# Optimization experiments

Hardware: AMD Instinct MI355X
Metric: run time of the kernel (lower is better)

## Reference

```python
import jax, jax.numpy as jnp
import numpy as np

DIM, NH, NKV, HD = 4096, 32, 8, 128
B, KV_LEN, WINDOW = 32, 4096, 4096
G = NH // NKV  # q heads per kv head (GQA group)


def setup_inputs() -> dict:
    key = jax.random.key(0)
    ks = jax.random.split(key, 7)
    s = 1.0 / np.sqrt(DIM)
    return {
        "x": jax.random.normal(ks[0], (1, 1, B, DIM), jnp.float32),
        "wqkv": jax.random.normal(ks[1], (DIM, DIM + 2 * NKV * HD), jnp.float32) * s,
        "wo": jax.random.normal(ks[2], (DIM, DIM), jnp.float32) * s,
        "rot_mat": jax.random.normal(ks[3], (HD, HD), jnp.float32) * (1.0 / np.sqrt(HD)),
        "cache_k": jax.random.normal(ks[4], (B, NKV, KV_LEN, HD), jnp.float32),
        "cache_v": jax.random.normal(ks[5], (B, NKV, KV_LEN, HD), jnp.float32),
        "attn_mask": jnp.zeros((1, NH, B, WINDOW), jnp.float32),
        "current_pos": 4095,
    }


def reference(x, wqkv, wo, rot_mat, cache_k, cache_v, attn_mask, current_pos):
    # fused QKV projection: (1,1,B,DIM) @ (DIM,6144) -> (1,1,B,6144)
    xqkv = x @ wqkv
    q = xqkv[..., : NH * HD].reshape(1, 1, B, NH, HD)
    k = xqkv[..., NH * HD : (NH + NKV) * HD].reshape(1, 1, B, NKV, HD)
    v = xqkv[..., (NH + NKV) * HD :].reshape(1, 1, B, NKV, HD)
    # nlp_create_qkv_heads layout: (seq, n_heads, batch, head_dim)
    q = jnp.transpose(q[:, 0], (0, 2, 1, 3))  # (1, NH, B, HD)
    k = jnp.transpose(k[:, 0], (0, 2, 1, 3))  # (1, NKV, B, HD)
    v = jnp.transpose(v[:, 0], (0, 2, 1, 3))  # (1, NKV, B, HD)
    # RoPE as matmul on last dim
    q = q @ rot_mat
    k = k @ rot_mat
    # KV-cache update at current_pos: cache is (B, NKV, KV_LEN, HD)
    cache_k = cache_k.at[:, :, current_pos, :].set(jnp.transpose(k[0], (1, 0, 2)))
    cache_v = cache_v.at[:, :, current_pos, :].set(jnp.transpose(v[0], (1, 0, 2)))
    # unpad valid region (padded to nearest 32, capped by sliding window)
    L = min(((current_pos + 1 + 31) // 32) * 32, WINDOW)
    keys = cache_k[:, :, :L]    # (B, NKV, L, HD)
    values = cache_v[:, :, :L]  # (B, NKV, L, HD)
    # grouped attention: q (1, NKV, G, B, HD) vs keys (B, NKV, L, HD)
    qg = q.reshape(1, NKV, G, B, HD)
    scores = jnp.einsum("qkgbd,bkld->qkgbl", qg, keys)  # (1,NKV,G,B,L)
    scores = scores.reshape(1, NH, B, L) / jnp.sqrt(jnp.float32(HD))
    scores = scores + attn_mask[..., :L]
    probs = jax.nn.softmax(scores, axis=-1)
    out = jnp.einsum("qkgbl,bkld->qkgbd", probs.reshape(1, NKV, G, B, L), values)
    out = out.reshape(1, NH, B, HD)
    # concatenate heads -> (1,1,B,DIM)
    out = jnp.transpose(out, (0, 2, 1, 3)).reshape(1, 1, B, NH * HD)
    return out @ wo
```

## Files before the change

### kernel.cpp

```cpp
#include <hip/hip_runtime.h>

#define BB 32
#define DIM 4096
#define NH 32
#define NKV 8
#define HD 128
#define KVLEN 4096
#define QKVC 6144
#define GQ 4
#define QKV_SPLITS 32
#define WO_SPLITS 32
#define ASPLIT 2
#define NT 32

typedef const __attribute__((address_space(1))) char gas_char;
typedef __attribute__((address_space(3))) char las_char;
#define GLL16(GP, LP) __builtin_amdgcn_global_load_lds((gas_char*)(GP), (las_char*)(LP), 16, 0, 0)

__global__ __launch_bounds__(256, 4) void k_qkv(const float* __restrict__ x,
                                                const float* __restrict__ w,
                                                float* __restrict__ part) {
    int j  = blockIdx.x * 256 + threadIdx.x;
    int d0 = blockIdx.y * (DIM / QKV_SPLITS);
    float acc[BB];
#pragma unroll
    for (int b = 0; b < BB; ++b) acc[b] = 0.f;
    for (int dd = d0; dd < d0 + DIM / QKV_SPLITS; dd += 16) {
        float wr[16];
#pragma unroll
        for (int k = 0; k < 16; ++k) wr[k] = w[(size_t)(dd + k) * QKVC + j];
#pragma unroll
        for (int b = 0; b < BB; ++b) {
            float4 xa = *(const float4*)&x[b * DIM + dd];
            float4 xb = *(const float4*)&x[b * DIM + dd + 4];
            float4 xc = *(const float4*)&x[b * DIM + dd + 8];
            float4 xd = *(const float4*)&x[b * DIM + dd + 12];
            float t = acc[b];
            t = fmaf(xa.x, wr[0],  t); t = fmaf(xa.y, wr[1],  t);
            t = fmaf(xa.z, wr[2],  t); t = fmaf(xa.w, wr[3],  t);
            t = fmaf(xb.x, wr[4],  t); t = fmaf(xb.y, wr[5],  t);
            t = fmaf(xb.z, wr[6],  t); t = fmaf(xb.w, wr[7],  t);
            t = fmaf(xc.x, wr[8],  t); t = fmaf(xc.y, wr[9],  t);
            t = fmaf(xc.z, wr[10], t); t = fmaf(xc.w, wr[11], t);
            t = fmaf(xd.x, wr[12], t); t = fmaf(xd.y, wr[13], t);
            t = fmaf(xd.z, wr[14], t); t = fmaf(xd.w, wr[15], t);
            acc[b] = t;
        }
    }
#pragma unroll
    for (int b = 0; b < BB; ++b)
        part[(size_t)blockIdx.y * (BB * QKVC) + (size_t)b * QKVC + j] = acc[b];
}

__global__ __launch_bounds__(256) void k_red(const float* __restrict__ src,
                                             float* __restrict__ dst,
                                             int parts, int n4) {
    int i = blockIdx.x * 256 + threadIdx.x;
    if (i >= n4) return;
    const float4* s4 = (const float4*)src;
    float4 a = s4[i];
    for (int p = 1; p < parts; ++p) {
        float4 b = s4[(size_t)p * n4 + i];
        a.x += b.x; a.y += b.y; a.z += b.z; a.w += b.w;
    }
    ((float4*)dst)[i] = a;
}

__global__ __launch_bounds__(128) void k_rot(const float* __restrict__ xqkv,
                                             const float* __restrict__ rot,
                                             float* __restrict__ qws,
                                             float* __restrict__ kws) {
    int c  = blockIdx.x;
    int b  = blockIdx.y;
    int dp = threadIdx.x;
    const float* row = &xqkv[(size_t)b * QKVC + c * HD];
    float acc = 0.f;
#pragma unroll 4
    for (int d = 0; d < HD; ++d) acc = fmaf(row[d], rot[d * HD + dp], acc);
    if (c < 32) {
        qws[((size_t)b * NH + c) * HD + dp] = acc;
    } else {
        int kvh = c - 32;
        kws[((size_t)b * NKV + kvh) * HD + dp] = acc;
    }
}

__global__ __launch_bounds__(256, 2) void k_attn(const float* __restrict__ ck,
                                                 const float* __restrict__ cv,
                                                 const float* __restrict__ qws,
                                                 const float* __restrict__ kws,
                                                 const float* __restrict__ xqkv,
                                                 const float* __restrict__ mask,
                                                 const int* __restrict__ curpos,
                                                 float* __restrict__ opart,
                                                 float2* __restrict__ stats) {
    __shared__ float Kl[2][64 * 128];
    __shared__ float mbuf[2][GQ * 64];
    __shared__ float ql[GQ][HD];
    __shared__ float pl[GQ * 64];
    __shared__ float rs[GQ];
    int bkv = blockIdx.x;
    int split = blockIdx.y;
    int b = bkv >> 3, kv = bkv & 7;
    int tid = threadIdx.x;
    int wv = tid >> 6, lane = tid & 63;
    int d4 = tid & 31, sub = tid >> 5;
    int lrh = lane >> 5;
    int sbyte = (lane & 31) << 4;
    int pos = *curpos;
    int L = min((((pos + 1) + 31) >> 5) << 5, KVLEN);
    int l0 = split * (NT * 64);
    int h = kv * GQ + wv;
    const float scale = 0.08838834764831845f;

    *(float2*)&ql[wv][lane * 2] = *(const float2*)&qws[((size_t)b * NH + h) * HD + lane * 2];

    float posdot = 0.f;
    {
        const float4* kwr = (const float4*)&kws[((size_t)b * NKV + kv) * HD];
        const float4* qr  = (const float4*)&qws[((size_t)b * NH + h) * HD];
#pragma unroll
        for (int i = 0; i < 32; ++i) {
            float4 a = kwr[i], c = qr[i];
            posdot += a.x * c.x + a.y * c.y + a.z * c.z + a.w * c.w;
        }
    }
    float4 vnew4 = *(const float4*)&xqkv[(size_t)b * QKVC + (size_t)(NH + NKV) * HD + kv * HD + d4 * 4];

    const char*   Ktile0 = (const char*)(ck + ((size_t)bkv * KVLEN + l0) * HD);
    const float4* Vt0    = (const float4*)(cv + ((size_t)bkv * KVLEN + l0) * HD);

#define STAGE_K(T, BUFI) do {                                                    \
        const char* kb_ = Ktile0 + (size_t)(T) * 32768;                          \
        _Pragma("unroll")                                                        \
        for (int i_ = 0; i_ < 8; ++i_) {                                         \
            int row_ = (i_ * 4 + wv) * 2 + lrh;                                  \
            int col_ = sbyte ^ ((row_ & 31) << 4);                               \
            GLL16(kb_ + (size_t)row_ * 512 + col_, &Kl[BUFI][(i_ * 4 + wv) * 256]); \
        }                                                                        \
    } while (0)

#define STAGE_M(T, BUFI) do {                                                    \
        int hh_ = lane >> 4, kk_ = lane & 15;                                    \
        const float* mg_ = mask + (((size_t)(kv * GQ + hh_) * BB + b) * KVLEN    \
                                   + l0 + (T) * 64 + kk_ * 4);                   \
        GLL16(mg_, &mbuf[BUFI][0]);                                              \
    } while (0)

    float m = -3.0e38f, lsum = 0.f;
    float4 acc[GQ];
#pragma unroll
    for (int gg = 0; gg < GQ; ++gg) acc[gg] = make_float4(0.f, 0.f, 0.f, 0.f);
    float4 vA[8], vB[8];

    STAGE_K(0, 0);
    if (wv == 0) STAGE_M(0, 0);
#pragma unroll
    for (int i = 0; i < 8; ++i) vA[i] = Vt0[(size_t)(sub * 8 + i) * 32 + d4];

#define TILE(T, BUFI, VC, VN) do {                                               \
        if ((T) < NT - 1) {                                                      \
            STAGE_K((T) + 1, (BUFI) ^ 1);                                        \
            if (wv == 0) STAGE_M((T) + 1, (BUFI) ^ 1);                           \
            _Pragma("unroll")                                                    \
            for (int i_ = 0; i_ < 8; ++i_)                                       \
                (VN)[i_] = Vt0[(size_t)(((T) + 1) * 64 + sub * 8 + i_) * 32 + d4]; \
            if (wv == 0) asm volatile("s_waitcnt vmcnt(17)" ::: "memory");       \
            else         asm volatile("s_waitcnt vmcnt(16)" ::: "memory");       \
        } else {                                                                 \
            asm volatile("s_waitcnt vmcnt(0)" ::: "memory");                     \
        }                                                                        \
        __builtin_amdgcn_s_barrier();                                            \
                                                   \
        int lk_ = l0 + (T) * 64 + lane;                                          \
        const char* klr_ = (const char*)&Kl[BUFI][0] + lane * 512;               \
        float sdot_ = 0.f;                                                       \
        _Pragma("unroll")                                                        \
        for (int dd_ = 0; dd_ < 32; ++dd_) {                                     \
            float4 kk4_ = *(const float4*)(klr_ + ((dd_ * 16) ^ sbyte));         \
            float4 qq4_ = *(const float4*)&ql[wv][dd_ * 4];                      \
            sdot_ += kk4_.x * qq4_.x + kk4_.y * qq4_.y                           \
                   + kk4_.z * qq4_.z + kk4_.w * qq4_.w;                          \
        }                                                                        \
        if (lk_ == pos) sdot_ = posdot;                                          \
        float s_ = sdot_ * scale + mbuf[BUFI][wv * 64 + lane];                   \
        if (lk_ >= L) s_ = -3.0e38f;                                             \
        float smax_ = s_;                                                        \
        _Pragma("unroll")                                                        \
        for (int off_ = 32; off_ > 0; off_ >>= 1)                                \
            smax_ = fmaxf(smax_, __shfl_xor(smax_, off_));                       \
        float mnew_ = fmaxf(m, smax_);                                           \
        float r_ = __expf(m - mnew_);                                            \
        float e_ = (lk_ < L) ? __expf(s_ - mnew_) : 0.f;                         \
        float esum_ = e_;                                                        \
        _Pragma("unroll")                                                        \
        for (int off_ = 32; off_ > 0; off_ >>= 1)                                \
            esum_ += __shfl_xor(esum_, off_);                                    \
        lsum = lsum * r_ + esum_;                                                \
        m = mnew_;                                                               \
        pl[wv * 64 + lane] = e_;                                                 \
        if (lane == 0) rs[wv] = r_;                                              \
        asm volatile("s_waitcnt lgkmcnt(0)" ::: "memory");                       \
        __builtin_amdgcn_s_barrier();                                            \
                              \
        int prow_ = pos - (l0 + (T) * 64);                                       \
        _Pragma("unroll")                                                        \
        for (int gg_ = 0; gg_ < GQ; ++gg_) {                                     \
            float rg_ = rs[gg_];                                                 \
            acc[gg_].x *= rg_; acc[gg_].y *= rg_;                                \
            acc[gg_].z *= rg_; acc[gg_].w *= rg_;                                \
        }                                                                        \
        _Pragma("unroll")                                                        \
        for (int i_ = 0; i_ < 8; ++i_) {                                         \
            float4 v_ = (sub * 8 + i_ == prow_) ? vnew4 : (VC)[i_];              \
            _Pragma("unroll")                                                    \
            for (int gg_ = 0; gg_ < GQ; ++gg_) {                                 \
                float p_ = pl[gg_ * 64 + sub * 8 + i_];                          \
                acc[gg_].x = fmaf(p_, v_.x, acc[gg_].x);                         \
                acc[gg_].y = fmaf(p_, v_.y, acc[gg_].y);                         \
                acc[gg_].z = fmaf(p_, v_.z, acc[gg_].z);                         \
                acc[gg_].w = fmaf(p_, v_.w, acc[gg_].w);                         \
            }                                                                    \
        }                                                                        \
    } while (0)

    for (int tt = 0; tt < NT; tt += 2) {
        TILE(tt,     0, vA, vB);
        TILE(tt + 1, 1, vB, vA);
    }

    if (lane == 0) stats[(bkv * GQ + wv) * ASPLIT + split] = make_float2(m, lsum);

    __syncthreads();
    float* red = &Kl[0][0];
#pragma unroll
    for (int gg = 0; gg < GQ; ++gg)
        *(float4*)&red[(sub * GQ + gg) * HD + d4 * 4] = acc[gg];
    __syncthreads();
#pragma unroll
    for (int rep = 0; rep < 2; ++rep) {
        int idx = rep * 256 + tid;
        int g2 = idx >> 7, d = idx & 127;
        float o = 0.f;
#pragma unroll
        for (int k = 0; k < 8; ++k) o += red[(k * GQ + g2) * HD + d];
        opart[(((size_t)split * 256 + bkv) * GQ + g2) * HD + d] = o;
    }
#undef TILE
#undef STAGE_K
#undef STAGE_M
}

__global__ __launch_bounds__(128) void k_merge(const float* __restrict__ opart,
                                               const float2* __restrict__ stats,
                                               float* __restrict__ attn) {
    int bkv = blockIdx.x;
    int d = threadIdx.x;
    int b = bkv >> 3, kv = bkv & 7;
#pragma unroll
    for (int g = 0; g < GQ; ++g) {
        float2 st[ASPLIT];
        float M = -3.0e38f;
#pragma unroll
        for (int s = 0; s < ASPLIT; ++s) {
            st[s] = stats[(bkv * GQ + g) * ASPLIT + s];
            M = fmaxf(M, st[s].x);
        }
        float Ltot = 0.f;
        float w[ASPLIT];
#pragma unroll
        for (int s = 0; s < ASPLIT; ++s) {
            w[s] = __expf(st[s].x - M);
            Ltot += st[s].y * w[s];
        }
        float inv = Ltot > 0.f ? 1.f / Ltot : 0.f;
        float o = 0.f;
#pragma unroll
        for (int s = 0; s < ASPLIT; ++s)
            o += opart[(((size_t)s * 256 + bkv) * GQ + g) * HD + d] * (w[s] * inv);
        attn[(size_t)b * DIM + (kv * GQ + g) * HD + d] = o;
    }
}

__global__ __launch_bounds__(256, 4) void k_wo(const float* __restrict__ attn,
                                               const float* __restrict__ wo,
                                               float* __restrict__ part) {
    int j  = blockIdx.x * 256 + threadIdx.x;
    int d0 = blockIdx.y * (DIM / WO_SPLITS);
    float acc[BB];
#pragma unroll
    for (int b = 0; b < BB; ++b) acc[b] = 0.f;
    for (int dd = d0; dd < d0 + DIM / WO_SPLITS; dd += 8) {
        float wr[8];
#pragma unroll
        for (int k = 0; k < 8; ++k) wr[k] = wo[(size_t)(dd + k) * DIM + j];
#pragma unroll
        for (int b = 0; b < BB; ++b) {
            float4 xa = *(const float4*)&attn[b * DIM + dd];
            float4 xb = *(const float4*)&attn[b * DIM + dd + 4];
            float t = acc[b];
            t = fmaf(xa.x, wr[0], t); t = fmaf(xa.y, wr[1], t);
            t = fmaf(xa.z, wr[2], t); t = fmaf(xa.w, wr[3], t);
            t = fmaf(xb.x, wr[4], t); t = fmaf(xb.y, wr[5], t);
            t = fmaf(xb.z, wr[6], t); t = fmaf(xb.w, wr[7], t);
            acc[b] = t;
        }
    }
#pragma unroll
    for (int b = 0; b < BB; ++b)
        part[(size_t)blockIdx.y * (BB * DIM) + (size_t)b * DIM + j] = acc[b];
}

extern "C" void kernel_launch(void* const* d_in, const int* in_sizes, int n_in,
                              void* d_out, int out_size, void* d_ws, size_t ws_size,
                              hipStream_t stream) {
    const float* x    = (const float*)d_in[0];
    const float* wqkv = (const float*)d_in[1];
    const float* wo   = (const float*)d_in[2];
    const float* rot  = (const float*)d_in[3];
    const float* ck   = (const float*)d_in[4];
    const float* cv   = (const float*)d_in[5];
    const float* mask = (const float*)d_in[6];
    const int* curpos = (const int*)d_in[7];
    float* out        = (float*)d_out;

    char* ws = (char*)d_ws;
    float*  xqkv_part = (float*)(ws);
    float*  xqkv      = (float*)(ws + 25165824);
    float*  qws       = (float*)(ws + 25952256);
    float*  kws       = (float*)(ws + 26476544);
    float*  opart     = (float*)(ws + 26607616);
    float2* stats     = (float2*)(ws + 28704768);
    float*  attn      = (float*)(ws + 28737536);
    float*  out_part  = (float*)(ws + 29261824);

    k_qkv  <<<dim3(QKVC / 256, QKV_SPLITS), 256, 0, stream>>>(x, wqkv, xqkv_part);
    k_red  <<<dim3(192),                    256, 0, stream>>>(xqkv_part, xqkv, QKV_SPLITS, BB * QKVC / 4);
    k_rot  <<<dim3(40, BB),                 128, 0, stream>>>(xqkv, rot, qws, kws);
    k_attn <<<dim3(BB * NKV, ASPLIT),       256, 0, stream>>>(ck, cv, qws, kws, xqkv, mask, curpos, opart, stats);
    k_merge<<<dim3(BB * NKV),               128, 0, stream>>>(opart, stats, attn);
    k_wo   <<<dim3(DIM / 256, WO_SPLITS),   256, 0, stream>>>(attn, wo, out_part);
    k_red  <<<dim3(128),                    256, 0, stream>>>(out_part, out, WO_SPLITS, BB * DIM / 4);
}
```

Before: 1.318 ms.

## Double attention block to 512 threads, splitting QK dot across wave pairs

The attention kernel now launches 512 threads per block. Each head's score dot product is split across two waves, each handling half of the head dimension, and the partials are combined through shared memory. Only four waves run the softmax, and K staging and V loads are spread over eight waves with half the per-thread register buffers. The aim is more memory-level parallelism and latency hiding for the bandwidth-bound KV-cache stream, at the cost of an extra barrier per tile and idle waves during softmax.

```diff
diff --git a/kernel.cpp b/kernel.cpp
--- a/kernel.cpp
+++ b/kernel.cpp
@@ -85,7 +85,7 @@
     }
 }
 
-__global__ __launch_bounds__(256, 2) void k_attn(const float* __restrict__ ck,
+__global__ __launch_bounds__(512, 4) void k_attn(const float* __restrict__ ck,
                                                  const float* __restrict__ cv,
                                                  const float* __restrict__ qws,
                                                  const float* __restrict__ kws,
@@ -97,28 +97,31 @@
     __shared__ float Kl[2][64 * 128];
     __shared__ float mbuf[2][GQ * 64];
     __shared__ float ql[GQ][HD];
+    __shared__ float pA[GQ][2][64];
     __shared__ float pl[GQ * 64];
     __shared__ float rs[GQ];
     int bkv = blockIdx.x;
     int split = blockIdx.y;
     int b = bkv >> 3, kv = bkv & 7;
     int tid = threadIdx.x;
-    int wv = tid >> 6, lane = tid & 63;
+    int w8 = tid >> 6, lane = tid & 63;
+    int hq = w8 >> 1, hf = w8 & 1;
+    int hf16 = hf * 16;
     int d4 = tid & 31, sub = tid >> 5;
     int lrh = lane >> 5;
     int sbyte = (lane & 31) << 4;
     int pos = *curpos;
     int L = min((((pos + 1) + 31) >> 5) << 5, KVLEN);
     int l0 = split * (NT * 64);
-    int h = kv * GQ + wv;
     const float scale = 0.08838834764831845f;
 
-    *(float2*)&ql[wv][lane * 2] = *(const float2*)&qws[((size_t)b * NH + h) * HD + lane * 2];
-
+    ql[tid >> 7][tid & 127] = qws[((size_t)b * NH + kv * GQ) * HD + tid];
+
+    int hp = w8 & 3;
     float posdot = 0.f;
     {
         const float4* kwr = (const float4*)&kws[((size_t)b * NKV + kv) * HD];
-        const float4* qr  = (const float4*)&qws[((size_t)b * NH + h) * HD];
+        const float4* qr  = (const float4*)&qws[((size_t)b * NH + kv * GQ + hp) * HD];
 #pragma unroll
         for (int i = 0; i < 32; ++i) {
             float4 a = kwr[i], c = qr[i];
@@ -133,10 +136,10 @@
 #define STAGE_K(T, BUFI) do {                                                    \
         const char* kb_ = Ktile0 + (size_t)(T) * 32768;                          \
         _Pragma("unroll")                                                        \
-        for (int i_ = 0; i_ < 8; ++i_) {                                         \
-            int row_ = (i_ * 4 + wv) * 2 + lrh;                                  \
+        for (int i_ = 0; i_ < 4; ++i_) {                                         \
+            int row_ = w8 * 8 + i_ * 2 + lrh;                                    \
             int col_ = sbyte ^ ((row_ & 31) << 4);                               \
-            GLL16(kb_ + (size_t)row_ * 512 + col_, &Kl[BUFI][(i_ * 4 + wv) * 256]); \
+            GLL16(kb_ + (size_t)row_ * 512 + col_, &Kl[BUFI][(w8 * 8 + i_ * 2) * 128]); \
         }                                                                        \
     } while (0)
 
@@ -147,61 +150,73 @@
         GLL16(mg_, &mbuf[BUFI][0]);                                              \
     } while (0)
 
+#define LOADV(T, VBUF) do {                                                      \
+        _Pragma("unroll")                                                        \
+        for (int i_ = 0; i_ < 4; ++i_)                                           \
+            (VBUF)[i_] = Vt0[(size_t)((T) * 64 + sub * 4 + i_) * 32 + d4];       \
+    } while (0)
+
     float m = -3.0e38f, lsum = 0.f;
     float4 acc[GQ];
 #pragma unroll
     for (int gg = 0; gg < GQ; ++gg) acc[gg] = make_float4(0.f, 0.f, 0.f, 0.f);
-    float4 vA[8], vB[8];
+    float4 vA[4], vB[4];
 
     STAGE_K(0, 0);
-    if (wv == 0) STAGE_M(0, 0);
-#pragma unroll
-    for (int i = 0; i < 8; ++i) vA[i] = Vt0[(size_t)(sub * 8 + i) * 32 + d4];
+    if (w8 == 0) STAGE_M(0, 0);
+    LOADV(0, vA);
+    asm volatile("s_waitcnt lgkmcnt(0)" ::: "memory");
 
 #define TILE(T, BUFI, VC, VN) do {                                               \
         if ((T) < NT - 1) {                                                      \
             STAGE_K((T) + 1, (BUFI) ^ 1);                                        \
-            if (wv == 0) STAGE_M((T) + 1, (BUFI) ^ 1);                           \
-            _Pragma("unroll")                                                    \
-            for (int i_ = 0; i_ < 8; ++i_)                                       \
-                (VN)[i_] = Vt0[(size_t)(((T) + 1) * 64 + sub * 8 + i_) * 32 + d4]; \
-            if (wv == 0) asm volatile("s_waitcnt vmcnt(17)" ::: "memory");       \
-            else         asm volatile("s_waitcnt vmcnt(16)" ::: "memory");       \
+            if (w8 == 0) STAGE_M((T) + 1, (BUFI) ^ 1);                           \
+            LOADV((T) + 1, VN);                                                  \
+            if (w8 == 0) asm volatile("s_waitcnt vmcnt(9)" ::: "memory");        \
+            else         asm volatile("s_waitcnt vmcnt(8)" ::: "memory");        \
         } else {                                                                 \
             asm volatile("s_waitcnt vmcnt(0)" ::: "memory");                     \
         }                                                                        \
-        __builtin_amdgcn_s_barrier();                                            \
-                                                   \
+        __builtin_amdgcn_s_barrier();                     \
+                           \
         int lk_ = l0 + (T) * 64 + lane;                                          \
         const char* klr_ = (const char*)&Kl[BUFI][0] + lane * 512;               \
-        float sdot_ = 0.f;                                                       \
-        _Pragma("unroll")                                                        \
-        for (int dd_ = 0; dd_ < 32; ++dd_) {                                     \
+        float pd_ = 0.f;                                                         \
+        _Pragma("unroll")                                                        \
+        for (int j_ = 0; j_ < 16; ++j_) {                                        \
+            int dd_ = hf16 + j_;                                                 \
             float4 kk4_ = *(const float4*)(klr_ + ((dd_ * 16) ^ sbyte));         \
-            float4 qq4_ = *(const float4*)&ql[wv][dd_ * 4];                      \
-            sdot_ += kk4_.x * qq4_.x + kk4_.y * qq4_.y                           \
-                   + kk4_.z * qq4_.z + kk4_.w * qq4_.w;                          \
-        }                                                                        \
-        if (lk_ == pos) sdot_ = posdot;                                          \
-        float s_ = sdot_ * scale + mbuf[BUFI][wv * 64 + lane];                   \
-        if (lk_ >= L) s_ = -3.0e38f;                                             \
-        float smax_ = s_;                                                        \
-        _Pragma("unroll")                                                        \
-        for (int off_ = 32; off_ > 0; off_ >>= 1)                                \
-            smax_ = fmaxf(smax_, __shfl_xor(smax_, off_));                       \
-        float mnew_ = fmaxf(m, smax_);                                           \
-        float r_ = __expf(m - mnew_);                                            \
-        float e_ = (lk_ < L) ? __expf(s_ - mnew_) : 0.f;                         \
-        float esum_ = e_;                                                        \
-        _Pragma("unroll")                                                        \
-        for (int off_ = 32; off_ > 0; off_ >>= 1)                                \
-            esum_ += __shfl_xor(esum_, off_);                                    \
-        lsum = lsum * r_ + esum_;                                                \
-        m = mnew_;                                                               \
-        pl[wv * 64 + lane] = e_;                                                 \
-        if (lane == 0) rs[wv] = r_;                                              \
+            float4 qq4_ = *(const float4*)&ql[hq][dd_ * 4];                      \
+            pd_ += kk4_.x * qq4_.x + kk4_.y * qq4_.y                             \
+                 + kk4_.z * qq4_.z + kk4_.w * qq4_.w;                            \
+        }                                                                        \
+        pA[hq][hf][lane] = pd_;                                                  \
         asm volatile("s_waitcnt lgkmcnt(0)" ::: "memory");                       \
-        __builtin_amdgcn_s_barrier();                                            \
+        __builtin_amdgcn_s_barrier();                  \
+                  \
+        if (w8 < 4) {                                                            \
+            float sdot_ = pA[w8][0][lane] + pA[w8][1][lane];                     \
+            if (lk_ == pos) sdot_ = posdot;                                      \
+            float s_ = sdot_ * scale + mbuf[BUFI][w8 * 64 + lane];               \
+            if (lk_ >= L) s_ = -3.0e38f;                                         \
+            float smax_ = s_;                                                    \
+            _Pragma("unroll")                                                    \
+            for (int off_ = 32; off_ > 0; off_ >>= 1)                            \
+                smax_ = fmaxf(smax_, __shfl_xor(smax_, off_));                   \
+            float mnew_ = fmaxf(m, smax_);                                       \
+            float r_ = __expf(m - mnew_);                                        \
+            float e_ = (lk_ < L) ? __expf(s_ - mnew_) : 0.f;                     \
+            float esum_ = e_;                                                    \
+            _Pragma("unroll")                                                    \
+            for (int off_ = 32; off_ > 0; off_ >>= 1)                            \
+                esum_ += __shfl_xor(esum_, off_);                                \
+            lsum = lsum * r_ + esum_;                                            \
+            m = mnew_;                                                           \
+            pl[w8 * 64 + lane] = e_;                                             \
+            if (lane == 0) rs[w8] = r_;                                          \
+        }                                                                        \
+        asm volatile("s_waitcnt lgkmcnt(0)" ::: "memory");                       \
+        __builtin_amdgcn_s_barrier();                     \
                               \
         int prow_ = pos - (l0 + (T) * 64);                                       \
         _Pragma("unroll")                                                        \
@@ -211,11 +226,11 @@
             acc[gg_].z *= rg_; acc[gg_].w *= rg_;                                \
         }                                                                        \
         _Pragma("unroll")                                                        \
-        for (int i_ = 0; i_ < 8; ++i_) {                                         \
-            float4 v_ = (sub * 8 + i_ == prow_) ? vnew4 : (VC)[i_];              \
+        for (int i_ = 0; i_ < 4; ++i_) {                                         \
+            float4 v_ = (sub * 4 + i_ == prow_) ? vnew4 : (VC)[i_];              \
             _Pragma("unroll")                                                    \
             for (int gg_ = 0; gg_ < GQ; ++gg_) {                                 \
-                float p_ = pl[gg_ * 64 + sub * 8 + i_];                          \
+                float p_ = pl[gg_ * 64 + sub * 4 + i_];                          \
                 acc[gg_].x = fmaf(p_, v_.x, acc[gg_].x);                         \
                 acc[gg_].y = fmaf(p_, v_.y, acc[gg_].y);                         \
                 acc[gg_].z = fmaf(p_, v_.z, acc[gg_].z);                         \
@@ -229,7 +244,8 @@
         TILE(tt + 1, 1, vB, vA);
     }
 
-    if (lane == 0) stats[(bkv * GQ + wv) * ASPLIT + split] = make_float2(m, lsum);
+    if (w8 < 4 && lane == 0)
+        stats[(bkv * GQ + w8) * ASPLIT + split] = make_float2(m, lsum);
 
     __syncthreads();
     float* red = &Kl[0][0];
@@ -237,16 +253,15 @@
     for (int gg = 0; gg < GQ; ++gg)
         *(float4*)&red[(sub * GQ + gg) * HD + d4 * 4] = acc[gg];
     __syncthreads();
-#pragma unroll
-    for (int rep = 0; rep < 2; ++rep) {
-        int idx = rep * 256 + tid;
-        int g2 = idx >> 7, d = idx & 127;
+    {
+        int g2 = tid >> 7, d = tid & 127;
         float o = 0.f;
 #pragma unroll
-        for (int k = 0; k < 8; ++k) o += red[(k * GQ + g2) * HD + d];
+        for (int k = 0; k < 16; ++k) o += red[(k * GQ + g2) * HD + d];
         opart[(((size_t)split * 256 + bkv) * GQ + g2) * HD + d] = o;
     }
 #undef TILE
+#undef LOADV
 #undef STAGE_K
 #undef STAGE_M
 }
@@ -337,7 +352,7 @@
     k_qkv  <<<dim3(QKVC / 256, QKV_SPLITS), 256, 0, stream>>>(x, wqkv, xqkv_part);
     k_red  <<<dim3(192),                    256, 0, stream>>>(xqkv_part, xqkv, QKV_SPLITS, BB * QKVC / 4);
     k_rot  <<<dim3(40, BB),                 128, 0, stream>>>(xqkv, rot, qws, kws);
-    k_attn <<<dim3(BB * NKV, ASPLIT),       256, 0, stream>>>(ck, cv, qws, kws, xqkv, mask, curpos, opart, stats);
+    k_attn <<<dim3(BB * NKV, ASPLIT),       512, 0, stream>>>(ck, cv, qws, kws, xqkv, mask, curpos, opart, stats);
     k_merge<<<dim3(BB * NKV),               128, 0, stream>>>(opart, stats, attn);
     k_wo   <<<dim3(DIM / 256, WO_SPLITS),   256, 0, stream>>>(attn, wo, out_part);
     k_red  <<<dim3(128),                    256, 0, stream>>>(out_part, out, WO_SPLITS, BB * DIM / 4);
```

New measurement: 1.481 ms. 1.12x slower.

## Software-pipeline attention tiles: overlap scores of tile T with PV of T-1

Applied to the files above, without the earlier changes.

Splits each attention tile into a score/softmax phase and a probability-times-V phase. The PV phase for tile T-1 now runs after the score phase for tile T, with double-buffered probability and rescale arrays. This cuts the barriers per tile from two to one and gives V loads a full tile of latency to arrive. It also splits the dot-product accumulators four ways for more ILP and drops the min-blocks launch bound, which may change register allocation and occupancy.

```diff
diff --git a/kernel.cpp b/kernel.cpp
--- a/kernel.cpp
+++ b/kernel.cpp
@@ -85,20 +85,20 @@
     }
 }
 
-__global__ __launch_bounds__(256, 2) void k_attn(const float* __restrict__ ck,
-                                                 const float* __restrict__ cv,
-                                                 const float* __restrict__ qws,
-                                                 const float* __restrict__ kws,
-                                                 const float* __restrict__ xqkv,
-                                                 const float* __restrict__ mask,
-                                                 const int* __restrict__ curpos,
-                                                 float* __restrict__ opart,
-                                                 float2* __restrict__ stats) {
+__global__ __launch_bounds__(256) void k_attn(const float* __restrict__ ck,
+                                              const float* __restrict__ cv,
+                                              const float* __restrict__ qws,
+                                              const float* __restrict__ kws,
+                                              const float* __restrict__ xqkv,
+                                              const float* __restrict__ mask,
+                                              const int* __restrict__ curpos,
+                                              float* __restrict__ opart,
+                                              float2* __restrict__ stats) {
     __shared__ float Kl[2][64 * 128];
     __shared__ float mbuf[2][GQ * 64];
     __shared__ float ql[GQ][HD];
-    __shared__ float pl[GQ * 64];
-    __shared__ float rs[GQ];
+    __shared__ float pl[2][GQ * 64];
+    __shared__ float rs[2][GQ];
     int bkv = blockIdx.x;
     int split = blockIdx.y;
     int b = bkv >> 3, kv = bkv & 7;
@@ -115,15 +115,23 @@
 
     *(float2*)&ql[wv][lane * 2] = *(const float2*)&qws[((size_t)b * NH + h) * HD + lane * 2];
 
-    float posdot = 0.f;
+    float posdot;
     {
         const float4* kwr = (const float4*)&kws[((size_t)b * NKV + kv) * HD];
         const float4* qr  = (const float4*)&qws[((size_t)b * NH + h) * HD];
-#pragma unroll
-        for (int i = 0; i < 32; ++i) {
-            float4 a = kwr[i], c = qr[i];
-            posdot += a.x * c.x + a.y * c.y + a.z * c.z + a.w * c.w;
-        }
+        float p0 = 0.f, p1 = 0.f, p2 = 0.f, p3 = 0.f;
+#pragma unroll
+        for (int i = 0; i < 32; i += 4) {
+            float4 a0 = kwr[i],     c0 = qr[i];
+            float4 a1 = kwr[i + 1], c1 = qr[i + 1];
+            float4 a2 = kwr[i + 2], c2 = qr[i + 2];
+            float4 a3 = kwr[i + 3], c3 = qr[i + 3];
+            p0 += a0.x * c0.x + a0.y * c0.y + a0.z * c0.z + a0.w * c0.w;
+            p1 += a1.x * c1.x + a1.y * c1.y + a1.z * c1.z + a1.w * c1.w;
+            p2 += a2.x * c2.x + a2.y * c2.y + a2.z * c2.z + a2.w * c2.w;
+            p3 += a3.x * c3.x + a3.y * c3.y + a3.z * c3.z + a3.w * c3.w;
+        }
+        posdot = (p0 + p1) + (p2 + p3);
     }
     float4 vnew4 = *(const float4*)&xqkv[(size_t)b * QKVC + (size_t)(NH + NKV) * HD + kv * HD + d4 * 4];
 
@@ -147,43 +155,41 @@
         GLL16(mg_, &mbuf[BUFI][0]);                                              \
     } while (0)
 
+#define LOADV(T, VBUF) do {                                                      \
+        _Pragma("unroll")                                                        \
+        for (int i_ = 0; i_ < 8; ++i_)                                           \
+            (VBUF)[i_] = Vt0[(size_t)((T) * 64 + sub * 8 + i_) * 32 + d4];       \
+    } while (0)
+
     float m = -3.0e38f, lsum = 0.f;
     float4 acc[GQ];
 #pragma unroll
     for (int gg = 0; gg < GQ; ++gg) acc[gg] = make_float4(0.f, 0.f, 0.f, 0.f);
     float4 vA[8], vB[8];
 
-    STAGE_K(0, 0);
-    if (wv == 0) STAGE_M(0, 0);
-#pragma unroll
-    for (int i = 0; i < 8; ++i) vA[i] = Vt0[(size_t)(sub * 8 + i) * 32 + d4];
-
-#define TILE(T, BUFI, VC, VN) do {                                               \
-        if ((T) < NT - 1) {                                                      \
-            STAGE_K((T) + 1, (BUFI) ^ 1);                                        \
-            if (wv == 0) STAGE_M((T) + 1, (BUFI) ^ 1);                           \
-            _Pragma("unroll")                                                    \
-            for (int i_ = 0; i_ < 8; ++i_)                                       \
-                (VN)[i_] = Vt0[(size_t)(((T) + 1) * 64 + sub * 8 + i_) * 32 + d4]; \
-            if (wv == 0) asm volatile("s_waitcnt vmcnt(17)" ::: "memory");       \
-            else         asm volatile("s_waitcnt vmcnt(16)" ::: "memory");       \
-        } else {                                                                 \
-            asm volatile("s_waitcnt vmcnt(0)" ::: "memory");                     \
-        }                                                                        \
-        __builtin_amdgcn_s_barrier();                                            \
-                                                   \
+#define PHASE_A(T) do {                                                          \
+        int par_ = (T) & 1;                                                      \
         int lk_ = l0 + (T) * 64 + lane;                                          \
-        const char* klr_ = (const char*)&Kl[BUFI][0] + lane * 512;               \
-        float sdot_ = 0.f;                                                       \
-        _Pragma("unroll")                                                        \
-        for (int dd_ = 0; dd_ < 32; ++dd_) {                                     \
-            float4 kk4_ = *(const float4*)(klr_ + ((dd_ * 16) ^ sbyte));         \
-            float4 qq4_ = *(const float4*)&ql[wv][dd_ * 4];                      \
-            sdot_ += kk4_.x * qq4_.x + kk4_.y * qq4_.y                           \
-                   + kk4_.z * qq4_.z + kk4_.w * qq4_.w;                          \
-        }                                                                        \
+        const char* klr_ = (const char*)&Kl[par_][0] + lane * 512;               \
+        float s0_ = 0.f, s1_ = 0.f, s2_ = 0.f, s3_ = 0.f;                        \
+        _Pragma("unroll")                                                        \
+        for (int dd_ = 0; dd_ < 32; dd_ += 4) {                                  \
+            float4 k0_ = *(const float4*)(klr_ + (((dd_ + 0) * 16) ^ sbyte));    \
+            float4 q0_ = *(const float4*)&ql[wv][(dd_ + 0) * 4];                 \
+            float4 k1_ = *(const float4*)(klr_ + (((dd_ + 1) * 16) ^ sbyte));    \
+            float4 q1_ = *(const float4*)&ql[wv][(dd_ + 1) * 4];                 \
+            float4 k2_ = *(const float4*)(klr_ + (((dd_ + 2) * 16) ^ sbyte));    \
+            float4 q2_ = *(const float4*)&ql[wv][(dd_ + 2) * 4];                 \
+            float4 k3_ = *(const float4*)(klr_ + (((dd_ + 3) * 16) ^ sbyte));    \
+            float4 q3_ = *(const float4*)&ql[wv][(dd_ + 3) * 4];                 \
+            s0_ += k0_.x * q0_.x + k0_.y * q0_.y + k0_.z * q0_.z + k0_.w * q0_.w; \
+            s1_ += k1_.x * q1_.x + k1_.y * q1_.y + k1_.z * q1_.z + k1_.w * q1_.w; \
+            s2_ += k2_.x * q2_.x + k2_.y * q2_.y + k2_.z * q2_.z + k2_.w * q2_.w; \
+            s3_ += k3_.x * q3_.x + k3_.y * q3_.y + k3_.z * q3_.z + k3_.w * q3_.w; \
+        }                                                                        \
+        float sdot_ = (s0_ + s1_) + (s2_ + s3_);                                 \
         if (lk_ == pos) sdot_ = posdot;                                          \
-        float s_ = sdot_ * scale + mbuf[BUFI][wv * 64 + lane];                   \
+        float s_ = sdot_ * scale + mbuf[par_][wv * 64 + lane];                   \
         if (lk_ >= L) s_ = -3.0e38f;                                             \
         float smax_ = s_;                                                        \
         _Pragma("unroll")                                                        \
@@ -198,15 +204,16 @@
             esum_ += __shfl_xor(esum_, off_);                                    \
         lsum = lsum * r_ + esum_;                                                \
         m = mnew_;                                                               \
-        pl[wv * 64 + lane] = e_;                                                 \
-        if (lane == 0) rs[wv] = r_;                                              \
-        asm volatile("s_waitcnt lgkmcnt(0)" ::: "memory");                       \
-        __builtin_amdgcn_s_barrier();                                            \
-                              \
-        int prow_ = pos - (l0 + (T) * 64);                                       \
+        pl[par_][wv * 64 + lane] = e_;                                           \
+        if (lane == 0) rs[par_][wv] = r_;                                        \
+    } while (0)
+
+#define PHASE_B(TB, VC) do {                                                     \
+        int parb_ = (TB) & 1;                                                    \
+        int prow_ = pos - (l0 + (TB) * 64);                                      \
         _Pragma("unroll")                                                        \
         for (int gg_ = 0; gg_ < GQ; ++gg_) {                                     \
-            float rg_ = rs[gg_];                                                 \
+            float rg_ = rs[parb_][gg_];                                          \
             acc[gg_].x *= rg_; acc[gg_].y *= rg_;                                \
             acc[gg_].z *= rg_; acc[gg_].w *= rg_;                                \
         }                                                                        \
@@ -215,7 +222,7 @@
             float4 v_ = (sub * 8 + i_ == prow_) ? vnew4 : (VC)[i_];              \
             _Pragma("unroll")                                                    \
             for (int gg_ = 0; gg_ < GQ; ++gg_) {                                 \
-                float p_ = pl[gg_ * 64 + sub * 8 + i_];                          \
+                float p_ = pl[parb_][gg_ * 64 + sub * 8 + i_];                   \
                 acc[gg_].x = fmaf(p_, v_.x, acc[gg_].x);                         \
                 acc[gg_].y = fmaf(p_, v_.y, acc[gg_].y);                         \
                 acc[gg_].z = fmaf(p_, v_.z, acc[gg_].z);                         \
@@ -224,12 +231,41 @@
         }                                                                        \
     } while (0)
 
-    for (int tt = 0; tt < NT; tt += 2) {
-        TILE(tt,     0, vA, vB);
-        TILE(tt + 1, 1, vB, vA);
-    }
+#define TILE(T, VC, VN) do {                                                     \
+        asm volatile("s_waitcnt vmcnt(8)" ::: "memory");                         \
+        asm volatile("s_waitcnt lgkmcnt(0)" ::: "memory");                       \
+        __builtin_amdgcn_s_barrier();                                            \
+        if ((T) < NT - 1) {                                                      \
+            STAGE_K((T) + 1, ((T) + 1) & 1);                                     \
+            if (wv == 0) STAGE_M((T) + 1, ((T) + 1) & 1);                        \
+        }                                                                        \
+        LOADV(T, VN);                                                            \
+        PHASE_A(T);                                                              \
+        PHASE_B((T) - 1, VC);                                                    \
+    } while (0)
+
+    STAGE_K(0, 0);
+    if (wv == 0) STAGE_M(0, 0);
+
+    asm volatile("s_waitcnt vmcnt(0)" ::: "memory");
+    asm volatile("s_waitcnt lgkmcnt(0)" ::: "memory");
+    __builtin_amdgcn_s_barrier();
+    STAGE_K(1, 1);
+    if (wv == 0) STAGE_M(1, 1);
+    LOADV(0, vA);
+    PHASE_A(0);
+
+    for (int tt = 1; tt < NT - 1; tt += 2) {
+        TILE(tt,     vA, vB);
+        TILE(tt + 1, vB, vA);
+    }
+    TILE(NT - 1, vA, vB);
 
     if (lane == 0) stats[(bkv * GQ + wv) * ASPLIT + split] = make_float2(m, lsum);
+
+    asm volatile("s_waitcnt lgkmcnt(0)" ::: "memory");
+    __builtin_amdgcn_s_barrier();
+    PHASE_B(NT - 1, vB);
 
     __syncthreads();
     float* red = &Kl[0][0];
@@ -247,6 +283,9 @@
         opart[(((size_t)split * 256 + bkv) * GQ + g2) * HD + d] = o;
     }
 #undef TILE
+#undef PHASE_A
+#undef PHASE_B
+#undef LOADV
 #undef STAGE_K
 #undef STAGE_M
 }
```

New measurement: 1.290 ms. 2.1% less time.
